# Optimization experiments

Hardware: AMD Instinct MI355X
Metric: run time of the kernel (lower is better)

Reference implementation:

```python
import jax, jax.numpy as jnp
import numpy as np

TEMP = 0.07
MAX_SAMPLES = 2048
RADIUS = 10
HARD_FRAC = 0.75
FG_LABEL = 1
B, C, H, W = 8, 64, 256, 256
BLOCK = 32

MAX_FG = MAX_SAMPLES // 2                      # 1024
NEG_BUDGET = MAX_SAMPLES - MAX_FG              # 1024
HARD_BUDGET = int(round(HARD_FRAC * NEG_BUDGET))  # 768
RAND_BUDGET = NEG_BUDGET - HARD_BUDGET         # 256


def setup_inputs() -> dict:
    key = jax.random.key(0)
    feats = jax.random.normal(key, (B, C, H, W), dtype=jnp.float32)
    # 32x32-block checkerboard labels: guarantees abundant fg / ring / interior-bg pools
    ii, jj = jnp.meshgrid(jnp.arange(H), jnp.arange(W), indexing='ij')
    lbl = (((ii // BLOCK) + (jj // BLOCK)) % 2).astype(jnp.int32)
    labels = jnp.broadcast_to(lbl, (B, H, W))
    return {"feats": feats, "labels": labels}


def _forward(feats, labels):
    Bn, Cn, Hn, Wn = feats.shape
    n_pix = Hn * Wn
    f_flat = feats.reshape(Bn, Cn, n_pix).transpose(0, 2, 1)  # [B, P, C]
    l_flat = labels.reshape(Bn, n_pix)

    fg = labels == FG_LABEL                                   # [B, H, W]
    k = 2 * RADIUS + 1
    # max-pool dilation of fg mask (kernel k, stride 1, pad RADIUS == SAME)
    dil = jax.lax.reduce_window(fg.astype(jnp.float32), -jnp.inf, jax.lax.max,
                                (1, k, k), (1, 1, 1), 'SAME') > 0.0
    fg_flat = fg.reshape(Bn, n_pix)
    bg_flat = ~fg_flat                                        # all pixels valid (no ignore)
    ring_flat = dil.reshape(Bn, n_pix) & ~fg_flat & bg_flat
    bgonly_flat = bg_flat & ~ring_flat

    def per_image(f, y, fgm, ringm, bgm, key):
        k1, k2, k3 = jax.random.split(key, 3)
        def pick(mask, kk, n):
            # random subset of n true positions (== randperm[:n] in distribution)
            s = jnp.where(mask, jax.random.uniform(kk, mask.shape), -1.0)
            return jax.lax.top_k(s, n)[1]
        idx = jnp.concatenate([pick(fgm, k1, MAX_FG),
                               pick(ringm, k2, HARD_BUDGET),
                               pick(bgm, k3, RAND_BUDGET)])    # [K]
        fs = f[idx]                                            # [K, C]
        ys = y[idx]
        fs = fs / jnp.maximum(jnp.linalg.norm(fs, axis=1, keepdims=True), 1e-12)
        logits = fs @ fs.T / TEMP                              # [K, K]
        logits = logits - jax.lax.stop_gradient(logits.max(axis=1, keepdims=True))
        eye = jnp.eye(MAX_SAMPLES, dtype=bool)
        pos = (ys[:, None] == ys[None, :]) & ~eye
        exp_l = jnp.exp(logits) * (~eye)
        denom = jnp.maximum(exp_l.sum(axis=1), 1e-8)
        pos_sum = jnp.maximum(jnp.where(pos, exp_l, 0.0).sum(axis=1), 1e-8)
        valid = pos.any(axis=1) & (ys == FG_LABEL)
        loss_terms = -jnp.log(pos_sum / denom)
        n_valid = jnp.maximum(valid.sum(), 1)
        return jnp.where(valid, loss_terms, 0.0).sum() / n_valid

    keys = jax.random.split(jax.random.key(1), Bn)
    losses = jax.vmap(per_image)(f_flat, l_flat, fg_flat, ring_flat, bgonly_flat, keys)
    return losses.mean()


def reference(feats, labels):
    return _forward(feats, labels)
```

## Files before the change

### kernel.cpp

```cpp
#include <hip/hip_runtime.h>
#include <stdint.h>

#define NPIX   65536
#define NIMG   8
#define NCH    64
#define KSEL   2048
#define NFG    1024
#define NRING  768
#define NBG    256
#define INV_TEMP 14.285714285714286f

__device__ __forceinline__ void tf2x32(uint32_t k0, uint32_t k1,
                                       uint32_t& x0, uint32_t& x1) {
  const uint32_t ks2 = k0 ^ k1 ^ 0x1BD11BDAu;
  x0 += k0; x1 += k1;
#define TF_RND(r) { x0 += x1; x1 = (x1 << (r)) | (x1 >> (32 - (r))); x1 ^= x0; }
  TF_RND(13) TF_RND(15) TF_RND(26) TF_RND(6)
  x0 += k1;  x1 += ks2 + 1u;
  TF_RND(17) TF_RND(29) TF_RND(16) TF_RND(24)
  x0 += ks2; x1 += k0 + 2u;
  TF_RND(13) TF_RND(15) TF_RND(26) TF_RND(6)
  x0 += k0;  x1 += k1 + 3u;
  TF_RND(17) TF_RND(29) TF_RND(16) TF_RND(24)
  x0 += k1;  x1 += ks2 + 4u;
  TF_RND(13) TF_RND(15) TF_RND(26) TF_RND(6)
  x0 += ks2; x1 += k0 + 5u;
#undef TF_RND
}

#define ZERO_F4 1552
__global__ __launch_bounds__(256) void dilate_h(const int* __restrict__ labels,
                                                uint8_t* __restrict__ hdil,
                                                float4* __restrict__ zregion,
                                                uint32_t* __restrict__ keys,
                                                float* __restrict__ out) {
  __shared__ int row[256];
  const int p = blockIdx.x * 256 + threadIdx.x;
  row[threadIdx.x] = labels[p];

  if (blockIdx.x < 7) {
    int t = blockIdx.x * 256 + threadIdx.x;
    if (t < ZERO_F4) zregion[t] = make_float4(0.f, 0.f, 0.f, 0.f);
  } else if (blockIdx.x == 7 && threadIdx.x == 0) {
    out[0] = 0.0f;
    for (int b = 0; b < NIMG; ++b) {
      uint32_t kb0 = 0u, kb1 = (uint32_t)b;
      tf2x32(0u, 1u, kb0, kb1);
      for (int g = 0; g < 3; ++g) {
        uint32_t x0 = 0u, x1 = (uint32_t)g;
        tf2x32(kb0, kb1, x0, x1);
        keys[(b * 3 + g) * 2 + 0] = x0;
        keys[(b * 3 + g) * 2 + 1] = x1;
      }
    }
  }
  __syncthreads();

  const int j = threadIdx.x;
  int lo = j - 10 > 0 ? j - 10 : 0;
  int hi = j + 10 < 255 ? j + 10 : 255;
  uint8_t v = 0;
  for (int jj = lo; jj <= hi; ++jj) v |= (row[jj] == 1);
  hdil[p] = v;
}

__global__ __launch_bounds__(256) void group_hash(const int* __restrict__ labels,
                                                  const uint8_t* __restrict__ hdil,
                                                  const uint32_t* __restrict__ keys,
                                                  uint32_t* __restrict__ mgrp,
                                                  uint32_t* __restrict__ hist) {
  __shared__ uint32_t lh[768];
  const int tid = threadIdx.x;
  for (int t = tid; t < 768; t += 256) lh[t] = 0;
  const int b = blockIdx.x >> 5;
  const int base = blockIdx.x * 2048;
  const uint32_t K00 = keys[b * 6 + 0], K01 = keys[b * 6 + 1];
  const uint32_t K10 = keys[b * 6 + 2], K11 = keys[b * 6 + 3];
  const uint32_t K20 = keys[b * 6 + 4], K21 = keys[b * 6 + 5];
  __syncthreads();

  #pragma unroll
  for (int k = 0; k < 8; ++k) {
    int p = base + k * 256 + tid;
    int pix = p & 65535;
    int i = pix >> 8, j = pix & 255;
    uint32_t grp;
    if (labels[p] == 1) {
      grp = 0;
    } else {
      int lo = i - 10 > 0 ? i - 10 : 0;
      int hi = i + 10 < 255 ? i + 10 : 255;
      uint8_t d = 0;
      for (int ii = lo; ii <= hi; ++ii) d |= hdil[(b << 16) + (ii << 8) + j];
      grp = d ? 1u : 2u;
    }
    uint32_t k0 = grp == 0 ? K00 : grp == 1 ? K10 : K20;
    uint32_t k1 = grp == 0 ? K01 : grp == 1 ? K11 : K21;
    uint32_t x0 = 0u, x1 = (uint32_t)pix;
    tf2x32(k0, k1, x0, x1);
    uint32_t m = (x0 ^ x1) >> 9;
    mgrp[p] = (m << 2) | grp;
    atomicAdd(&lh[grp * 256 + (m >> 15)], 1u);
  }
  __syncthreads();
  for (int t = tid; t < 768; t += 256)
    if (lh[t]) atomicAdd(&hist[b * 768 + t], lh[t]);
}

__global__ __launch_bounds__(256) void topk_emit(const uint32_t* __restrict__ mgrp,
                                                 const uint32_t* __restrict__ hist,
                                                 uint32_t* __restrict__ TG,
                                                 uint32_t* __restrict__ cnt,
                                                 uint32_t* __restrict__ candcnt,
                                                 unsigned long long* __restrict__ cand,
                                                 int* __restrict__ idx_out) {
  __shared__ uint32_t hh[768];
  __shared__ uint32_t sT[3], loc[3], lbd[3], basA[3], basB[3];
  const int tid = threadIdx.x;
  const int b = blockIdx.x >> 5;
  const int base = blockIdx.x * 2048;
  for (int t = tid; t < 768; t += 256) hh[t] = hist[b * 768 + t];
  if (tid < 3) { loc[tid] = 0; lbd[tid] = 0; }
  __syncthreads();

  if (tid < 3) {
    uint32_t nsel = tid == 0 ? NFG : tid == 1 ? NRING : NBG;
    const uint32_t* h = hh + tid * 256;
    uint32_t cum = 0; int T = 255;
    for (; T > 0; --T) {
      uint32_t c = h[T];
      if (cum + c >= nsel) break;
      cum += c;
    }
    sT[tid] = (uint32_t)T;
    if ((blockIdx.x & 31) == 0) {
      TG[(b * 3 + tid) * 2] = (uint32_t)T;
      TG[(b * 3 + tid) * 2 + 1] = cum;
    }
  }
  __syncthreads();
  const uint32_t T0 = sT[0], T1 = sT[1], T2 = sT[2];

  #pragma unroll
  for (int k = 0; k < 8; ++k) {
    uint32_t v = mgrp[base + k * 256 + tid];
    uint32_t g = v & 3u, bin = v >> 17;
    uint32_t T = g == 0 ? T0 : g == 1 ? T1 : T2;
    if (bin > T) atomicAdd(&loc[g], 1u);
    else if (bin == T) atomicAdd(&lbd[g], 1u);
  }
  __syncthreads();
  if (tid < 3) {
    basA[tid] = atomicAdd(&cnt[b * 3 + tid], loc[tid]);
    basB[tid] = atomicAdd(&candcnt[b * 3 + tid], lbd[tid]);
    loc[tid] = 0; lbd[tid] = 0;
  }
  __syncthreads();

  #pragma unroll
  for (int k = 0; k < 8; ++k) {
    int p = base + k * 256 + tid;
    uint32_t v = mgrp[p];
    uint32_t g = v & 3u, bin = v >> 17;
    uint32_t T = g == 0 ? T0 : g == 1 ? T1 : T2;
    int pix = p & 65535;
    if (bin > T) {
      uint32_t o = atomicAdd(&loc[g], 1u);
      int seg = g == 0 ? 0 : g == 1 ? NFG : (NFG + NRING);
      idx_out[b * KSEL + seg + (int)(basA[g] + o)] = pix;
    } else if (bin == T) {
      uint32_t o = atomicAdd(&lbd[g], 1u);
      uint32_t c = basB[g] + o;
      uint32_t m = v >> 2;
      if (c < 1024u)
        cand[(b * 3 + g) * 1024 + c] = ((unsigned long long)m << 16) | (uint32_t)pix;
    }
  }
}

__global__ __launch_bounds__(256) void topk_rank(const uint32_t* __restrict__ TG,
                                                 const uint32_t* __restrict__ candcnt,
                                                 const unsigned long long* __restrict__ cand,
                                                 int* __restrict__ idx_out) {
  __shared__ unsigned long long cb[1024];
  const int task = blockIdx.x;
  const int b = task / 3, g = task % 3;
  const int nsel = g == 0 ? NFG : g == 1 ? NRING : NBG;
  const int seg  = g == 0 ? 0 : g == 1 ? NFG : (NFG + NRING);
  const uint32_t G = TG[task * 2 + 1];
  const int r = nsel - (int)G;
  const int c = (int)(candcnt[task] < 1024u ? candcnt[task] : 1024u);
  for (int i = threadIdx.x; i < c; i += 256) cb[i] = cand[task * 1024 + i];
  __syncthreads();
  for (int i = threadIdx.x; i < c; i += 256) {
    unsigned long long me = cb[i];
    uint32_t mm = (uint32_t)(me >> 16), pi = (uint32_t)(me & 0xFFFFu);
    int rank = 0;
    for (int j = 0; j < c; ++j) {
      unsigned long long o = cb[j];
      uint32_t om = (uint32_t)(o >> 16), op = (uint32_t)(o & 0xFFFFu);
      if (om > mm || (om == mm && op < pi)) ++rank;
    }
    if (rank < r) idx_out[b * KSEL + seg + (int)G + rank] = (int)pi;
  }
}

__global__ __launch_bounds__(256) void gather_t(const float* __restrict__ feats,
                                                const int* __restrict__ idx,
                                                float* __restrict__ fsT) {
  __shared__ float tile[32 * 65];
  __shared__ float ssb[8 * 32];
  const int tid = threadIdx.x;
  const int a = tid & 31, q = tid >> 5;
  const int w = blockIdx.x * 32 + a;
  const int img = blockIdx.x >> 6;
  const int pix = idx[w];
  const float* fb = feats + ((size_t)img * NCH + q * 8) * NPIX + pix;
  float ss = 0.f;
  #pragma unroll
  for (int k = 0; k < 8; ++k) {
    float v = fb[(size_t)k * NPIX];
    tile[a * 65 + q * 8 + k] = v;
    ss += v * v;
  }
  ssb[q * 32 + a] = ss;
  __syncthreads();

  const int a2 = tid & 31;
  const int j = (blockIdx.x & 63) * 32 + a2;
  float tot = 0.f;
  #pragma unroll
  for (int q2 = 0; q2 < 8; ++q2) tot += ssb[q2 * 32 + a2];
  float scale = 1.0f / fmaxf(sqrtf(tot), 1e-12f);
  float* dst = fsT + (size_t)img * NCH * KSEL;
  #pragma unroll
  for (int k = 0; k < 8; ++k) {
    int c = (tid >> 5) + 8 * k;
    dst[(size_t)c * KSEL + j] = tile[a2 * 65 + c] * scale;
  }
}

#define LTA 8
__global__ __launch_bounds__(256) void loss_main(const float* __restrict__ fsT,
                                                 float* __restrict__ out) {
  const int img = blockIdx.x & 7;
  const int a0 = (blockIdx.x >> 3) * LTA;
  const float* F = fsT + (size_t)img * NCH * KSEL;
  const float4* F4 = (const float4*)F;
  const int tid = threadIdx.x;

  __shared__ float As[LTA * 64];
  __shared__ float redD[4][LTA], redP[4][LTA], terms[LTA];
  for (int t = tid; t < LTA * 64; t += 256) {
    int a = t & 7, c = t >> 3;
    As[a * 64 + c] = F[(size_t)c * KSEL + a0 + a];
  }
  __syncthreads();

  float acc[LTA][8];
  #pragma unroll
  for (int a = 0; a < LTA; ++a)
    #pragma unroll
    for (int jj = 0; jj < 8; ++jj) acc[a][jj] = 0.f;

  #pragma unroll 4
  for (int c = 0; c < 64; ++c) {
    float4 b0 = F4[c * 512 + tid];
    float4 b1 = F4[c * 512 + 256 + tid];
    #pragma unroll
    for (int a = 0; a < LTA; ++a) {
      float av = As[a * 64 + c];
      acc[a][0] += av * b0.x; acc[a][1] += av * b0.y;
      acc[a][2] += av * b0.z; acc[a][3] += av * b0.w;
      acc[a][4] += av * b1.x; acc[a][5] += av * b1.y;
      acc[a][6] += av * b1.z; acc[a][7] += av * b1.w;
    }
  }

  float pD[LTA], pP[LTA];
  const int jb = 4 * tid;
  #pragma unroll
  for (int a = 0; a < LTA; ++a) {
    const int ag = a0 + a;
    float p = 0.f, d = 0.f;
    #pragma unroll
    for (int jj = 0; jj < 4; ++jj) {
      float e = __expf(acc[a][jj] * INV_TEMP);
      if (jb + jj == ag) e = 0.f;
      p += e;
    }
    #pragma unroll
    for (int jj = 0; jj < 4; ++jj) d += __expf(acc[a][4 + jj] * INV_TEMP);
    pD[a] = d + p;
    pP[a] = p;
  }

  #pragma unroll
  for (int o = 32; o > 0; o >>= 1) {
    #pragma unroll
    for (int a = 0; a < LTA; ++a) {
      pD[a] += __shfl_xor(pD[a], o);
      pP[a] += __shfl_xor(pP[a], o);
    }
  }
  if ((tid & 63) == 0) {
    #pragma unroll
    for (int a = 0; a < LTA; ++a) {
      redD[tid >> 6][a] = pD[a];
      redP[tid >> 6][a] = pP[a];
    }
  }
  __syncthreads();
  if (tid < LTA) {
    float d = redD[0][tid] + redD[1][tid] + redD[2][tid] + redD[3][tid];
    float p = redP[0][tid] + redP[1][tid] + redP[2][tid] + redP[3][tid];
    d = fmaxf(d, 1e-8f); p = fmaxf(p, 1e-8f);
    terms[tid] = __logf(d) - __logf(p);
  }
  __syncthreads();
  if (tid == 0) {
    float s = 0.f;
    #pragma unroll
    for (int a = 0; a < LTA; ++a) s += terms[a];
    atomicAdd(out, s * (1.0f / (NFG * NIMG)));
  }
}

extern "C" void kernel_launch(void* const* d_in, const int* in_sizes, int n_in,
                              void* d_out, int out_size, void* d_ws, size_t ws_size,
                              hipStream_t stream) {
  const float* feats = (const float*)d_in[0];
  const int* labels  = (const int*)d_in[1];
  float* out = (float*)d_out;

  char* ws = (char*)d_ws;
  uint8_t*  hdil    = (uint8_t*)(ws);
  uint32_t* mgrp    = (uint32_t*)(ws + 524288);
  uint32_t* keys    = (uint32_t*)(ws + 2621440);
  uint32_t* TG      = (uint32_t*)(ws + 2621696);
  uint32_t* hist    = (uint32_t*)(ws + 2621952);
  uint32_t* cnt     = (uint32_t*)(ws + 2646528);
  uint32_t* candcnt = (uint32_t*)(ws + 2646656);
  unsigned long long* cand = (unsigned long long*)(ws + 2646784);
  int*      idx     = (int*)(ws + 2843392);
  float*    fsT     = (float*)(ws + 2908928);

  hipLaunchKernelGGL(dilate_h, dim3(NIMG * 256), dim3(256), 0, stream,
                     labels, hdil, (float4*)hist, keys, out);
  hipLaunchKernelGGL(group_hash, dim3(NIMG * 32), dim3(256), 0, stream,
                     labels, hdil, keys, mgrp, hist);
  hipLaunchKernelGGL(topk_emit, dim3(NIMG * 32), dim3(256), 0, stream,
                     mgrp, hist, TG, cnt, candcnt, cand, idx);
  hipLaunchKernelGGL(topk_rank, dim3(24), dim3(256), 0, stream,
                     TG, candcnt, cand, idx);
  hipLaunchKernelGGL(gather_t, dim3((NIMG * KSEL) / 32), dim3(256), 0, stream,
                     feats, idx, fsT);
  hipLaunchKernelGGL(loss_main, dim3(NIMG * (NFG / LTA)), dim3(256), 0, stream,
                     fsT, out);
}
```

Measured before the change: 278.1 us.

## Bit-pack dilation, fuse rank into gather, widen loss tile

Replaces the byte-per-pixel horizontal dilation with a ballot-based 64-bit packed mask. The packed mask is dilated horizontally by shifts and vertically by OR-ing rows, and the hash kernel reads bits instead of scanning 21 rows of bytes per pixel. The separate 24-block top-k rank kernel is merged into the gather kernel: blocks whose window overlaps the boundary bucket recompute the ranks locally, which removes a launch and a serialized tiny kernel but duplicates the O(c^2) rank work across several blocks. The loss kernel's row tile grows from 8 to 16 with less unrolling, which halves its grid and raises register pressure.

```diff
diff --git a/kernel.cpp b/kernel.cpp
--- a/kernel.cpp
+++ b/kernel.cpp
@@ -29,19 +29,21 @@
 }
 
 #define ZERO_F4 1552
-__global__ __launch_bounds__(256) void dilate_h(const int* __restrict__ labels,
-                                                uint8_t* __restrict__ hdil,
-                                                float4* __restrict__ zregion,
-                                                uint32_t* __restrict__ keys,
-                                                float* __restrict__ out) {
-  __shared__ int row[256];
-  const int p = blockIdx.x * 256 + threadIdx.x;
-  row[threadIdx.x] = labels[p];
-
-  if (blockIdx.x < 7) {
-    int t = blockIdx.x * 256 + threadIdx.x;
-    if (t < ZERO_F4) zregion[t] = make_float4(0.f, 0.f, 0.f, 0.f);
-  } else if (blockIdx.x == 7 && threadIdx.x == 0) {
+__global__ __launch_bounds__(1024) void dilate_pack(const int* __restrict__ labels,
+                                                    uint64_t* __restrict__ fgw,
+                                                    uint64_t* __restrict__ dilw,
+                                                    float4* __restrict__ zregion,
+                                                    uint32_t* __restrict__ keys,
+                                                    float* __restrict__ out) {
+  __shared__ uint64_t fgs[336], hds[336];
+  const int tid = threadIdx.x;
+  const int img = blockIdx.x >> 2;
+  const int r0 = (blockIdx.x & 3) * 64;
+
+  if (blockIdx.x == 0) {
+    for (int t = tid; t < ZERO_F4; t += 1024)
+      zregion[t] = make_float4(0.f, 0.f, 0.f, 0.f);
+  } else if (blockIdx.x == 1 && tid == 0) {
     out[0] = 0.0f;
     for (int b = 0; b < NIMG; ++b) {
       uint32_t kb0 = 0u, kb1 = (uint32_t)b;
@@ -54,26 +56,59 @@
       }
     }
   }
-  __syncthreads();
-
-  const int j = threadIdx.x;
-  int lo = j - 10 > 0 ? j - 10 : 0;
-  int hi = j + 10 < 255 ? j + 10 : 255;
-  uint8_t v = 0;
-  for (int jj = lo; jj <= hi; ++jj) v |= (row[jj] == 1);
-  hdil[p] = v;
-}
-
-__global__ __launch_bounds__(256) void group_hash(const int* __restrict__ labels,
-                                                  const uint8_t* __restrict__ hdil,
-                                                  const uint32_t* __restrict__ keys,
-                                                  uint32_t* __restrict__ mgrp,
-                                                  uint32_t* __restrict__ hist) {
+
+  #pragma unroll
+  for (int it = 0; it < 21; ++it) {
+    int li = it * 1024 + tid;
+    int hr = r0 - 10 + (li >> 8);
+    int col = li & 255;
+    bool bit = false;
+    if (hr >= 0 && hr < 256) bit = (labels[(img << 16) + (hr << 8) + col] == 1);
+    uint64_t m = __ballot(bit);
+    if ((tid & 63) == 0) fgs[li >> 6] = m;
+  }
+  __syncthreads();
+
+  for (int w = tid; w < 336; w += 1024) {
+    int wc = w & 3;
+    uint64_t x = fgs[w];
+    uint64_t L = wc > 0 ? fgs[w - 1] : 0ull;
+    uint64_t R = wc < 3 ? fgs[w + 1] : 0ull;
+    uint64_t acc = x;
+    #pragma unroll
+    for (int s = 1; s <= 10; ++s) {
+      acc |= (x << s) | (L >> (64 - s));
+      acc |= (x >> s) | (R << (64 - s));
+    }
+    hds[w] = acc;
+  }
+  __syncthreads();
+
+  for (int w = tid; w < 256; w += 1024) {
+    int r = w >> 2, wc = w & 3;
+    int gr = r0 + r;
+    uint64_t acc = 0ull;
+    #pragma unroll
+    for (int dr = 0; dr <= 20; ++dr) acc |= hds[(r + dr) * 4 + wc];
+    fgw[img * 1024 + gr * 4 + wc]  = fgs[(r + 10) * 4 + wc];
+    dilw[img * 1024 + gr * 4 + wc] = acc;
+  }
+}
+
+__global__ __launch_bounds__(256) void hash_hist(const uint64_t* __restrict__ fgw,
+                                                 const uint64_t* __restrict__ dilw,
+                                                 const uint32_t* __restrict__ keys,
+                                                 uint32_t* __restrict__ mgrp,
+                                                 uint32_t* __restrict__ hist) {
   __shared__ uint32_t lh[768];
+  __shared__ uint64_t fgl[32], dll[32];
   const int tid = threadIdx.x;
   for (int t = tid; t < 768; t += 256) lh[t] = 0;
   const int b = blockIdx.x >> 5;
   const int base = blockIdx.x * 2048;
+  const int w0 = (blockIdx.x & 31) * 32;
+  if (tid < 32) fgl[tid] = fgw[b * 1024 + w0 + tid];
+  else if (tid < 64) dll[tid - 32] = dilw[b * 1024 + w0 + tid - 32];
   const uint32_t K00 = keys[b * 6 + 0], K01 = keys[b * 6 + 1];
   const uint32_t K10 = keys[b * 6 + 2], K11 = keys[b * 6 + 3];
   const uint32_t K20 = keys[b * 6 + 4], K21 = keys[b * 6 + 5];
@@ -81,25 +116,18 @@
 
   #pragma unroll
   for (int k = 0; k < 8; ++k) {
-    int p = base + k * 256 + tid;
-    int pix = p & 65535;
-    int i = pix >> 8, j = pix & 255;
-    uint32_t grp;
-    if (labels[p] == 1) {
-      grp = 0;
-    } else {
-      int lo = i - 10 > 0 ? i - 10 : 0;
-      int hi = i + 10 < 255 ? i + 10 : 255;
-      uint8_t d = 0;
-      for (int ii = lo; ii <= hi; ++ii) d |= hdil[(b << 16) + (ii << 8) + j];
-      grp = d ? 1u : 2u;
-    }
+    int off = k * 256 + tid;
+    int pix = (base + off) & 65535;
+    int lw = off >> 6, bp = off & 63;
+    uint32_t fgbit = (uint32_t)((fgl[lw] >> bp) & 1ull);
+    uint32_t dilbit = (uint32_t)((dll[lw] >> bp) & 1ull);
+    uint32_t grp = fgbit ? 0u : (dilbit ? 1u : 2u);
     uint32_t k0 = grp == 0 ? K00 : grp == 1 ? K10 : K20;
     uint32_t k1 = grp == 0 ? K01 : grp == 1 ? K11 : K21;
     uint32_t x0 = 0u, x1 = (uint32_t)pix;
     tf2x32(k0, k1, x0, x1);
     uint32_t m = (x0 ^ x1) >> 9;
-    mgrp[p] = (m << 2) | grp;
+    mgrp[base + off] = (m << 2) | grp;
     atomicAdd(&lh[grp * 256 + (m >> 15)], 1u);
   }
   __syncthreads();
@@ -178,69 +206,78 @@
   }
 }
 
-__global__ __launch_bounds__(256) void topk_rank(const uint32_t* __restrict__ TG,
-                                                 const uint32_t* __restrict__ candcnt,
-                                                 const unsigned long long* __restrict__ cand,
-                                                 int* __restrict__ idx_out) {
+#define GA 16
+__global__ __launch_bounds__(256) void gather_rank_t(
+    const float* __restrict__ feats, const int* __restrict__ idx,
+    const uint32_t* __restrict__ TG, const uint32_t* __restrict__ candcnt,
+    const unsigned long long* __restrict__ cand, float* __restrict__ fsT) {
+  __shared__ float tile[GA * 65];
+  __shared__ float ssb[16 * GA];
+  __shared__ int lidx[GA];
   __shared__ unsigned long long cb[1024];
-  const int task = blockIdx.x;
-  const int b = task / 3, g = task % 3;
-  const int nsel = g == 0 ? NFG : g == 1 ? NRING : NBG;
-  const int seg  = g == 0 ? 0 : g == 1 ? NFG : (NFG + NRING);
+  const int tid = threadIdx.x;
+  const int img = blockIdx.x >> 7;
+  const int win = (blockIdx.x & 127) * GA;
+  int seg, segoff, nsel;
+  if (win < NFG)               { seg = 0; segoff = 0;            nsel = NFG; }
+  else if (win < NFG + NRING)  { seg = 1; segoff = NFG;          nsel = NRING; }
+  else                         { seg = 2; segoff = NFG + NRING;  nsel = NBG; }
+  const int task = img * 3 + seg;
   const uint32_t G = TG[task * 2 + 1];
-  const int r = nsel - (int)G;
-  const int c = (int)(candcnt[task] < 1024u ? candcnt[task] : 1024u);
-  for (int i = threadIdx.x; i < c; i += 256) cb[i] = cand[task * 1024 + i];
-  __syncthreads();
-  for (int i = threadIdx.x; i < c; i += 256) {
-    unsigned long long me = cb[i];
-    uint32_t mm = (uint32_t)(me >> 16), pi = (uint32_t)(me & 0xFFFFu);
-    int rank = 0;
-    for (int j = 0; j < c; ++j) {
-      unsigned long long o = cb[j];
-      uint32_t om = (uint32_t)(o >> 16), op = (uint32_t)(o & 0xFFFFu);
-      if (om > mm || (om == mm && op < pi)) ++rank;
-    }
-    if (rank < r) idx_out[b * KSEL + seg + (int)G + rank] = (int)pi;
-  }
-}
-
-__global__ __launch_bounds__(256) void gather_t(const float* __restrict__ feats,
-                                                const int* __restrict__ idx,
-                                                float* __restrict__ fsT) {
-  __shared__ float tile[32 * 65];
-  __shared__ float ssb[8 * 32];
-  const int tid = threadIdx.x;
-  const int a = tid & 31, q = tid >> 5;
-  const int w = blockIdx.x * 32 + a;
-  const int img = blockIdx.x >> 6;
-  const int pix = idx[w];
-  const float* fb = feats + ((size_t)img * NCH + q * 8) * NPIX + pix;
+  const int poslo = win - segoff;
+
+  if (tid < GA) {
+    if ((uint32_t)(poslo + tid) < G)
+      lidx[tid] = idx[img * KSEL + win + tid];
+  }
+  const bool needRank = (uint32_t)(poslo + GA) > G;
+  if (needRank) {
+    const int c = (int)(candcnt[task] < 1024u ? candcnt[task] : 1024u);
+    const int r = nsel - (int)G;
+    for (int i = tid; i < c; i += 256) cb[i] = cand[task * 1024 + i];
+    __syncthreads();
+    for (int i = tid; i < c; i += 256) {
+      unsigned long long me = cb[i];
+      uint32_t mm = (uint32_t)(me >> 16), pi = (uint32_t)(me & 0xFFFFu);
+      int rank = 0;
+      for (int j = 0; j < c; ++j) {
+        unsigned long long o = cb[j];
+        uint32_t om = (uint32_t)(o >> 16), op = (uint32_t)(o & 0xFFFFu);
+        if (om > mm || (om == mm && op < pi)) ++rank;
+      }
+      if (rank < r) {
+        int slot = (int)G + rank - poslo;
+        if (slot >= 0 && slot < GA) lidx[slot] = (int)pi;
+      }
+    }
+  }
+  __syncthreads();
+
+  const int a = tid & 15, q = tid >> 4;
+  const int pix = lidx[a];
+  const float* fb = feats + ((size_t)img * NCH + q * 4) * NPIX + pix;
   float ss = 0.f;
   #pragma unroll
-  for (int k = 0; k < 8; ++k) {
+  for (int k = 0; k < 4; ++k) {
     float v = fb[(size_t)k * NPIX];
-    tile[a * 65 + q * 8 + k] = v;
+    tile[a * 65 + q * 4 + k] = v;
     ss += v * v;
   }
-  ssb[q * 32 + a] = ss;
-  __syncthreads();
-
-  const int a2 = tid & 31;
-  const int j = (blockIdx.x & 63) * 32 + a2;
+  ssb[q * GA + a] = ss;
+  __syncthreads();
   float tot = 0.f;
   #pragma unroll
-  for (int q2 = 0; q2 < 8; ++q2) tot += ssb[q2 * 32 + a2];
+  for (int q2 = 0; q2 < 16; ++q2) tot += ssb[q2 * GA + a];
   float scale = 1.0f / fmaxf(sqrtf(tot), 1e-12f);
-  float* dst = fsT + (size_t)img * NCH * KSEL;
-  #pragma unroll
-  for (int k = 0; k < 8; ++k) {
-    int c = (tid >> 5) + 8 * k;
-    dst[(size_t)c * KSEL + j] = tile[a2 * 65 + c] * scale;
-  }
-}
-
-#define LTA 8
+  float* dst = fsT + (size_t)img * NCH * KSEL + win;
+  #pragma unroll
+  for (int k = 0; k < 4; ++k) {
+    int c = q * 4 + k;
+    dst[(size_t)c * KSEL + a] = tile[a * 65 + c] * scale;
+  }
+}
+
+#define LTA 16
 __global__ __launch_bounds__(256) void loss_main(const float* __restrict__ fsT,
                                                  float* __restrict__ out) {
   const int img = blockIdx.x & 7;
@@ -252,7 +289,7 @@
   __shared__ float As[LTA * 64];
   __shared__ float redD[4][LTA], redP[4][LTA], terms[LTA];
   for (int t = tid; t < LTA * 64; t += 256) {
-    int a = t & 7, c = t >> 3;
+    int a = t & 15, c = t >> 4;
     As[a * 64 + c] = F[(size_t)c * KSEL + a0 + a];
   }
   __syncthreads();
@@ -263,7 +300,7 @@
     #pragma unroll
     for (int jj = 0; jj < 8; ++jj) acc[a][jj] = 0.f;
 
-  #pragma unroll 4
+  #pragma unroll 2
   for (int c = 0; c < 64; ++c) {
     float4 b0 = F4[c * 512 + tid];
     float4 b1 = F4[c * 512 + 256 + tid];
@@ -334,27 +371,26 @@
   float* out = (float*)d_out;
 
   char* ws = (char*)d_ws;
-  uint8_t*  hdil    = (uint8_t*)(ws);
+  uint64_t* fgw     = (uint64_t*)(ws);
+  uint64_t* dilw    = (uint64_t*)(ws + 65536);
+  uint32_t* keys    = (uint32_t*)(ws + 131072);
+  uint32_t* TG      = (uint32_t*)(ws + 131328);
+  uint32_t* hist    = (uint32_t*)(ws + 131584);
+  uint32_t* cnt     = (uint32_t*)(ws + 156160);
+  uint32_t* candcnt = (uint32_t*)(ws + 156288);
+  unsigned long long* cand = (unsigned long long*)(ws + 156416);
+  int*      idx     = (int*)(ws + 353024);
   uint32_t* mgrp    = (uint32_t*)(ws + 524288);
-  uint32_t* keys    = (uint32_t*)(ws + 2621440);
-  uint32_t* TG      = (uint32_t*)(ws + 2621696);
-  uint32_t* hist    = (uint32_t*)(ws + 2621952);
-  uint32_t* cnt     = (uint32_t*)(ws + 2646528);
-  uint32_t* candcnt = (uint32_t*)(ws + 2646656);
-  unsigned long long* cand = (unsigned long long*)(ws + 2646784);
-  int*      idx     = (int*)(ws + 2843392);
-  float*    fsT     = (float*)(ws + 2908928);
-
-  hipLaunchKernelGGL(dilate_h, dim3(NIMG * 256), dim3(256), 0, stream,
-                     labels, hdil, (float4*)hist, keys, out);
-  hipLaunchKernelGGL(group_hash, dim3(NIMG * 32), dim3(256), 0, stream,
-                     labels, hdil, keys, mgrp, hist);
+  float*    fsT     = (float*)(ws + 2621440);
+
+  hipLaunchKernelGGL(dilate_pack, dim3(32), dim3(1024), 0, stream,
+                     labels, fgw, dilw, (float4*)hist, keys, out);
+  hipLaunchKernelGGL(hash_hist, dim3(NIMG * 32), dim3(256), 0, stream,
+                     fgw, dilw, keys, mgrp, hist);
   hipLaunchKernelGGL(topk_emit, dim3(NIMG * 32), dim3(256), 0, stream,
                      mgrp, hist, TG, cnt, candcnt, cand, idx);
-  hipLaunchKernelGGL(topk_rank, dim3(24), dim3(256), 0, stream,
-                     TG, candcnt, cand, idx);
-  hipLaunchKernelGGL(gather_t, dim3((NIMG * KSEL) / 32), dim3(256), 0, stream,
-                     feats, idx, fsT);
+  hipLaunchKernelGGL(gather_rank_t, dim3((NIMG * KSEL) / GA), dim3(256), 0, stream,
+                     feats, idx, TG, candcnt, cand, fsT);
   hipLaunchKernelGGL(loss_main, dim3(NIMG * (NFG / LTA)), dim3(256), 0, stream,
                      fsT, out);
 }
```

Result: faster. 250.4 us (-10.0%).
